# Performance work log

Measured on AMD Instinct MI355X. Metric: run time of the kernel, lower is better.

## Reference

```python
import jax, jax.numpy as jnp
import numpy as np

N = 20000      # nodes per batched graph
E = 320000     # directed edges per batched graph
F_IN = 128     # num_features
H = 256        # nhid == each gnn filter
G = 128        # number of graphs in batch


def setup_inputs() -> dict:
    key = jax.random.key(0)
    ks = jax.random.split(key, 24)

    def glorot(k, shape):
        fan_in, fan_out = shape[0], shape[1]
        limit = np.sqrt(6.0 / (fan_in + fan_out)).astype(np.float32)
        return jax.random.uniform(k, shape, jnp.float32, -limit, limit)

    inp = {
        'x1': jax.random.normal(ks[0], (N, F_IN), jnp.float32),
        'x2': jax.random.normal(ks[1], (N, F_IN), jnp.float32),
        'edge_index1': jax.random.randint(ks[2], (2, E), 0, N),
        'edge_index2': jax.random.randint(ks[3], (2, E), 0, N),
        'batch1': jnp.sort(jax.random.randint(ks[4], (N,), 0, G)),
        'batch2': jnp.sort(jax.random.randint(ks[5], (N,), 0, G)),
        # GCN layer weights (shared between the two graphs, as in the module)
        'W0': glorot(ks[6], (F_IN, H)), 'b0': jnp.zeros((H,), jnp.float32),
        'W1': glorot(ks[7], (H, H)),    'b1': jnp.zeros((H,), jnp.float32),
        'W2': glorot(ks[8], (H, H)),    'b2': jnp.zeros((H,), jnp.float32),
        # MLP head: nhid*2 -> nhid -> nhid//2 -> 1
        'lw0': glorot(ks[9], (2 * H, H)),      'lb0': jnp.zeros((H,), jnp.float32),
        'lw1': glorot(ks[10], (H, H // 2)),    'lb1': jnp.zeros((H // 2,), jnp.float32),
        'lw2': glorot(ks[11], (H // 2, 1)),    'lb2': jnp.zeros((1,), jnp.float32),
    }
    return inp


def _gcn_conv(x, src, dst, W, b, n):
    """PyG GCNConv: x' = D^-1/2 (A + I) D^-1/2 (x W) + b (self-loops added)."""
    x = x @ W                                      # [N, out]
    loop = jnp.arange(n)
    s = jnp.concatenate([src, loop])               # sources incl. self-loops
    d = jnp.concatenate([dst, loop])               # targets incl. self-loops
    deg = jax.ops.segment_sum(jnp.ones(s.shape, jnp.float32), d, num_segments=n)
    dinv = jnp.where(deg > 0, deg ** -0.5, 0.0)
    norm = dinv[s] * dinv[d]                       # [E+N]
    out = jax.ops.segment_sum(x[s] * norm[:, None], d, num_segments=n)
    return out + b


def _encode(x, edge_index, batch, params):
    src, dst = edge_index[0], edge_index[1]
    n = x.shape[0]
    for (W, b) in params:
        # conv -> relu -> dropout(eval: identity)
        x = jax.nn.relu(_gcn_conv(x, src, dst, W, b, n))
    # global_add_pool
    return jax.ops.segment_sum(x, batch, num_segments=G)   # [G, H]


def reference(x1, x2, W0, b0, W1, b1, W2, b2,
              lw0, lb0, lw1, lb1, lw2, lb2,
              edge_index1, edge_index2, batch1, batch2):
    params = ((W0, b0), (W1, b1), (W2, b2))
    g1 = _encode(x1, edge_index1, batch1, params)
    g2 = _encode(x2, edge_index2, batch2, params)
    scores = jnp.concatenate([g1, g2], axis=1)              # [G, 2H]
    h = jax.nn.relu(scores @ lw0 + lb0)
    h = jax.nn.relu(h @ lw1 + lb1)
    return jax.nn.sigmoid(h @ lw2 + lb2).reshape(-1)        # [G]
```

## Files before the change

### kernel.cpp

```cpp
#include <hip/hip_runtime.h>
#include <hip/hip_bf16.h>
#include <math.h>

#define HD 256
#define GB 128

typedef __attribute__((ext_vector_type(8))) short bf16x8;
typedef __attribute__((ext_vector_type(4))) float f32x4;

__device__ __forceinline__ float bf2f(unsigned short u) {
  return __uint_as_float(((unsigned int)u) << 16);
}
__device__ __forceinline__ unsigned short f2bf(float f) {
  unsigned int u = __float_as_uint(f);
  unsigned int r = u + 0x7FFFu + ((u >> 16) & 1u);
  return (unsigned short)(r >> 16);
}

__global__ void k_prep3(const float* __restrict__ W0, const float* __restrict__ W1,
                        const float* __restrict__ W2, unsigned short* __restrict__ Wt0,
                        unsigned short* __restrict__ Wt1, unsigned short* __restrict__ Wt2) {
  int i = blockIdx.x * blockDim.x + threadIdx.x;
  const float* W; unsigned short* Wt; int j;
  if (i < 32768)       { W = W0; Wt = Wt0; j = i; }
  else if (i < 98304)  { W = W1; Wt = Wt1; j = i - 32768; }
  else if (i < 163840) { W = W2; Wt = Wt2; j = i - 98304; }
  else return;
  int k = j >> 8, c = j & 255;
  Wt[(((size_t)(k >> 3) * HD) + c) * 8 + (k & 7)] = f2bf(W[(size_t)k * HD + c]);
}

__global__ void k_cvt2(const float4* __restrict__ in1, const float4* __restrict__ in2,
                       ushort4* __restrict__ out, int n4) {
  int i = blockIdx.x * blockDim.x + threadIdx.x;
  if (i >= 2 * n4) return;
  float4 v = (i < n4) ? in1[i] : in2[i - n4];
  ushort4 o;
  o.x = f2bf(v.x); o.y = f2bf(v.y); o.z = f2bf(v.z); o.w = f2bf(v.w);
  out[i] = o;
}

__global__ void k_zero(float* __restrict__ scores, int* __restrict__ deg, int ns, int nd) {
  int i = blockIdx.x * blockDim.x + threadIdx.x;
  if (i < ns) scores[i] = 0.f;
  else if (i < ns + nd) deg[i - ns] = 0;
}

__global__ void k_deg2(const int* __restrict__ dst1, const int* __restrict__ dst2,
                       int* __restrict__ deg, int e, int n0) {
  int i = blockIdx.x * blockDim.x + threadIdx.x;
  if (i >= 2 * e) return;
  int d = (i < e) ? dst1[i] : (dst2[i - e] + n0);
  atomicAdd(&deg[d], 1);
}

__global__ __launch_bounds__(256) void k_scan_a(const int* __restrict__ deg,
                                                int* __restrict__ partial, int n) {
  __shared__ int sh[256];
  int i = blockIdx.x * 256 + threadIdx.x;
  int v = (i < n) ? deg[i] : 0;
  sh[threadIdx.x] = v;
  __syncthreads();
#pragma unroll
  for (int off = 128; off; off >>= 1) {
    if (threadIdx.x < off) sh[threadIdx.x] += sh[threadIdx.x + off];
    __syncthreads();
  }
  if (threadIdx.x == 0) partial[blockIdx.x] = sh[0];
}

__global__ __launch_bounds__(256) void k_scan_b(int* __restrict__ partial, int nb,
                                                int* __restrict__ row_ptr, int n, int e_total) {
  __shared__ int sh[256];
  int t = threadIdx.x;
  int v = (t < nb) ? partial[t] : 0;
  sh[t] = v;
  __syncthreads();
#pragma unroll
  for (int off = 1; off < 256; off <<= 1) {
    int u = (t >= off) ? sh[t - off] : 0;
    __syncthreads();
    sh[t] += u;
    __syncthreads();
  }
  if (t < nb) partial[t] = sh[t] - v;
  if (t == 0) row_ptr[n] = e_total;
}

__global__ __launch_bounds__(256) void k_scan_c(const int* __restrict__ deg,
                                                const int* __restrict__ partial,
                                                int* __restrict__ row_ptr,
                                                float* __restrict__ dinv,
                                                int* __restrict__ cursor, int n) {
  __shared__ int sh[256];
  int i = blockIdx.x * 256 + threadIdx.x;
  int t = threadIdx.x;
  int v = (i < n) ? deg[i] : 0;
  sh[t] = v;
  __syncthreads();
#pragma unroll
  for (int off = 1; off < 256; off <<= 1) {
    int u = (t >= off) ? sh[t - off] : 0;
    __syncthreads();
    sh[t] += u;
    __syncthreads();
  }
  if (i < n) {
    row_ptr[i] = sh[t] - v + partial[blockIdx.x];
    dinv[i] = rsqrtf((float)(v + 1));
    cursor[i] = 0;
  }
}

__global__ void k_build2(const int* __restrict__ ei1, const int* __restrict__ ei2,
                         const float* __restrict__ dinv, const int* __restrict__ row_ptr,
                         int* __restrict__ cursor, int2* __restrict__ csr, int e, int n0) {
  int i = blockIdx.x * blockDim.x + threadIdx.x;
  if (i >= 2 * e) return;
  int s, d;
  if (i < e) { s = ei1[i];          d = ei1[i + e]; }
  else       { s = ei2[i - e] + n0; d = ei2[i] + n0; }
  int pos = atomicAdd(&cursor[d], 1);
  int idx = row_ptr[d] + pos;
  csr[idx] = make_int2(s, __float_as_int(dinv[s] * dinv[d]));
}

template<bool BR>
__global__ __launch_bounds__(256) void k_gemm_bf(const unsigned short* __restrict__ A,
                                                 const unsigned short* __restrict__ Wt,
                                                 const float* __restrict__ bias,
                                                 unsigned short* __restrict__ C,
                                                 int K) {
  const int w = threadIdx.x >> 6;
  const int lane = threadIdx.x & 63;
  const int bm = blockIdx.x * 64 + w * 16;
  const int bn = blockIdx.y * 128;
  const int row = bm + (lane & 15);
  const int kg0 = lane >> 4;
  f32x4 acc[8];
#pragma unroll
  for (int i = 0; i < 8; ++i) acc[i] = (f32x4){0.f, 0.f, 0.f, 0.f};

  const unsigned short* arow = A + (size_t)row * K + kg0 * 8;
  for (int k0 = 0; k0 < K; k0 += 32) {
    bf16x8 a = *(const bf16x8*)(arow + k0);
    const unsigned short* bbase =
        Wt + (((size_t)((k0 >> 3) + kg0) * HD) + bn + (lane & 15)) * 8;
#pragma unroll
    for (int nt = 0; nt < 8; ++nt) {
      bf16x8 b = *(const bf16x8*)(bbase + (size_t)nt * 16 * 8);
      acc[nt] = __builtin_amdgcn_mfma_f32_16x16x32_bf16(a, b, acc[nt], 0, 0, 0);
    }
  }
  const int crow = bm + (lane >> 4) * 4;
  const int ccol = bn + (lane & 15);
#pragma unroll
  for (int nt = 0; nt < 8; ++nt) {
    float bb = BR ? bias[ccol + nt * 16] : 0.f;
#pragma unroll
    for (int r = 0; r < 4; ++r) {
      float v = acc[nt][r];
      if (BR) v = fmaxf(v + bb, 0.f);
      C[(size_t)(crow + r) * HD + ccol + nt * 16] = f2bf(v);
    }
  }
}

template<int FB>
__device__ __forceinline__ void load_row(const unsigned short* p, float (&f)[FB]) {
  if constexpr (FB == 4) {
    ushort4 v = *(const ushort4*)p;
    f[0] = bf2f(v.x); f[1] = bf2f(v.y); f[2] = bf2f(v.z); f[3] = bf2f(v.w);
  } else {
    ushort2 v = *(const ushort2*)p;
    f[0] = bf2f(v.x); f[1] = bf2f(v.y);
  }
}

template<int FB, bool BR>
__global__ __launch_bounds__(256) void k_gath(const unsigned short* __restrict__ xw,
                                              const int* __restrict__ row_ptr,
                                              const int2* __restrict__ csr,
                                              const float* __restrict__ dinv,
                                              const float* __restrict__ bias,
                                              unsigned short* __restrict__ out, int n) {
  constexpr int F = FB * 64;
  int node = (blockIdx.x * blockDim.x + threadIdx.x) >> 6;
  int lane = threadIdx.x & 63;
  if (node >= n) return;
  float di = dinv[node];
  float c = di * di;
  float self[FB], acc0[FB], acc1[FB];
  load_row<FB>(xw + (size_t)node * F + lane * FB, self);
#pragma unroll
  for (int q = 0; q < FB; ++q) { acc0[q] = c * self[q]; acc1[q] = 0.f; }

  int e = row_ptr[node], end = row_ptr[node + 1];
  while (e < end) {
    int cnt = min(end - e, 64);
    int2 ew = make_int2(0, 0);
    if (lane < cnt) ew = csr[e + lane];
    int j = 0;
    for (; j + 4 <= cnt; j += 4) {
      int s0 = __shfl(ew.x, j + 0), s1 = __shfl(ew.x, j + 1);
      int s2 = __shfl(ew.x, j + 2), s3 = __shfl(ew.x, j + 3);
      float w0 = __int_as_float(__shfl(ew.y, j + 0));
      float w1 = __int_as_float(__shfl(ew.y, j + 1));
      float w2 = __int_as_float(__shfl(ew.y, j + 2));
      float w3 = __int_as_float(__shfl(ew.y, j + 3));
      float r0[FB], r1[FB], r2[FB], r3[FB];
      load_row<FB>(xw + (size_t)s0 * F + lane * FB, r0);
      load_row<FB>(xw + (size_t)s1 * F + lane * FB, r1);
      load_row<FB>(xw + (size_t)s2 * F + lane * FB, r2);
      load_row<FB>(xw + (size_t)s3 * F + lane * FB, r3);
#pragma unroll
      for (int q = 0; q < FB; ++q) {
        acc0[q] = fmaf(w0, r0[q], acc0[q]);
        acc1[q] = fmaf(w1, r1[q], acc1[q]);
        acc0[q] = fmaf(w2, r2[q], acc0[q]);
        acc1[q] = fmaf(w3, r3[q], acc1[q]);
      }
    }
    for (; j < cnt; ++j) {
      int s0 = __shfl(ew.x, j);
      float w0 = __int_as_float(__shfl(ew.y, j));
      float r0[FB];
      load_row<FB>(xw + (size_t)s0 * F + lane * FB, r0);
#pragma unroll
      for (int q = 0; q < FB; ++q) acc0[q] = fmaf(w0, r0[q], acc0[q]);
    }
    e += cnt;
  }
  unsigned short o[FB];
#pragma unroll
  for (int q = 0; q < FB; ++q) {
    float v = acc0[q] + acc1[q];
    if (BR) v = fmaxf(v + bias[lane * FB + q], 0.f);
    o[q] = f2bf(v);
  }
  if constexpr (FB == 4) {
    ushort4 ov; ov.x = o[0]; ov.y = o[1]; ov.z = o[2]; ov.w = o[3];
    *(ushort4*)(out + (size_t)node * F + lane * FB) = ov;
  } else {
    ushort2 ov; ov.x = o[0]; ov.y = o[1];
    *(ushort2*)(out + (size_t)node * F + lane * FB) = ov;
  }
}

__global__ __launch_bounds__(256) void k_pool4(const unsigned short* __restrict__ h,
                                               const int* __restrict__ batch1,
                                               const int* __restrict__ batch2,
                                               float* __restrict__ scores,
                                               int n, int n0) {
  int wave = (blockIdx.x * blockDim.x + threadIdx.x) >> 6;
  int lane = threadIdx.x & 63;
  int beg = wave * 32;
  if (beg >= n) return;
  int end = min(beg + 32, n);
  bool g1 = beg >= n0;
  const int* bat = g1 ? batch2 : batch1;
  int boff = g1 ? n0 : 0;
  int coff = g1 ? HD : 0;
  float ax = 0.f, ay = 0.f, az = 0.f, aw = 0.f;
  int cur = bat[beg - boff];
  for (int i = beg; i < end; ++i) {
    int b = bat[i - boff];
    if (b != cur) {
      float* srow = &scores[(size_t)cur * 512 + coff + lane * 4];
      atomicAdd(&srow[0], ax); atomicAdd(&srow[1], ay);
      atomicAdd(&srow[2], az); atomicAdd(&srow[3], aw);
      ax = ay = az = aw = 0.f;
      cur = b;
    }
    ushort4 v = reinterpret_cast<const ushort4*>(h + (size_t)i * HD)[lane];
    ax += bf2f(v.x); ay += bf2f(v.y); az += bf2f(v.z); aw += bf2f(v.w);
  }
  float* srow = &scores[(size_t)cur * 512 + coff + lane * 4];
  atomicAdd(&srow[0], ax); atomicAdd(&srow[1], ay);
  atomicAdd(&srow[2], az); atomicAdd(&srow[3], aw);
}

__global__ __launch_bounds__(256) void k_head_a(const float* __restrict__ scores,
                                                const float* __restrict__ lw0,
                                                const float* __restrict__ lb0,
                                                float* __restrict__ h1) {
  __shared__ float s_in[512];
  __shared__ float part[4][64];
  const int r = blockIdx.x, ct = blockIdx.y;
  const int t = threadIdx.x;
  s_in[t]       = scores[(size_t)r * 512 + t];
  s_in[t + 256] = scores[(size_t)r * 512 + t + 256];
  __syncthreads();
  const int l = t & 63, w = t >> 6;
  const int col = ct * 64 + l;
  float acc = 0.f;
  const float* wp = lw0 + (size_t)(w * 128) * 256 + col;
  const float* sp = s_in + w * 128;
#pragma unroll 8
  for (int k = 0; k < 128; ++k) acc = fmaf(sp[k], wp[(size_t)k * 256], acc);
  part[w][l] = acc;
  __syncthreads();
  if (t < 64) {
    float v = part[0][t] + part[1][t] + part[2][t] + part[3][t] + lb0[ct * 64 + t];
    h1[(size_t)r * 256 + ct * 64 + t] = fmaxf(v, 0.f);
  }
}

__global__ __launch_bounds__(256) void k_head_b(const float* __restrict__ h1,
                                                const float* __restrict__ lw1,
                                                const float* __restrict__ lb1,
                                                const float* __restrict__ lw2,
                                                const float* __restrict__ lb2,
                                                float* __restrict__ out) {
  __shared__ float s_in[256];
  __shared__ float part[2][128];
  __shared__ float s_h2[128];
  __shared__ float red[4];
  const int r = blockIdx.x;
  const int t = threadIdx.x;
  s_in[t] = h1[(size_t)r * 256 + t];
  __syncthreads();
  const int l = t & 127, w = t >> 7;
  float acc = 0.f;
  const float* wp = lw1 + (size_t)(w * 128) * 128 + l;
  const float* sp = s_in + w * 128;
#pragma unroll 8
  for (int k = 0; k < 128; ++k) acc = fmaf(sp[k], wp[(size_t)k * 128], acc);
  part[w][l] = acc;
  __syncthreads();
  if (t < 128) s_h2[t] = fmaxf(part[0][t] + part[1][t] + lb1[t], 0.f);
  __syncthreads();
  float p = (t < 128) ? s_h2[t] * lw2[t] : 0.f;
#pragma unroll
  for (int off = 32; off; off >>= 1) p += __shfl_down(p, off);
  if ((t & 63) == 0) red[t >> 6] = p;
  __syncthreads();
  if (t == 0) {
    float z = red[0] + red[1] + red[2] + red[3] + lb2[0];
    out[r] = 1.f / (1.f + expf(-z));
  }
}

extern "C" void kernel_launch(void* const* d_in, const int* in_sizes, int n_in,
                              void* d_out, int out_size, void* d_ws, size_t ws_size,
                              hipStream_t stream) {
  const float* x1 = (const float*)d_in[0];
  const float* x2 = (const float*)d_in[1];
  const int* ei1 = (const int*)d_in[2];
  const int* ei2 = (const int*)d_in[3];
  const int* batch1 = (const int*)d_in[4];
  const int* batch2 = (const int*)d_in[5];
  const float* W0 = (const float*)d_in[6];  const float* b0 = (const float*)d_in[7];
  const float* W1 = (const float*)d_in[8];  const float* b1 = (const float*)d_in[9];
  const float* W2 = (const float*)d_in[10]; const float* b2 = (const float*)d_in[11];
  const float* lw0 = (const float*)d_in[12]; const float* lb0 = (const float*)d_in[13];
  const float* lw1 = (const float*)d_in[14]; const float* lb1 = (const float*)d_in[15];
  const float* lw2 = (const float*)d_in[16]; const float* lb2 = (const float*)d_in[17];
  float* out = (float*)d_out;

  const int N = in_sizes[0] / 128;
  const int E = in_sizes[2] / 2;
  const int N2 = 2 * N, E2 = 2 * E;
  const int NB = (N2 + 255) / 256;

  char* p = (char*)d_ws;
  unsigned short* x_bf = (unsigned short*)p; p += (size_t)N2 * 128 * 2;
  unsigned short* aggx = (unsigned short*)p; p += (size_t)N2 * 128 * 2;
  unsigned short* buf0 = (unsigned short*)p; p += (size_t)N2 * HD * 2;
  unsigned short* buf1 = (unsigned short*)p; p += (size_t)N2 * HD * 2;
  unsigned short* Wt0  = (unsigned short*)p; p += (size_t)128 * HD * 2;
  unsigned short* Wt1  = (unsigned short*)p; p += (size_t)HD * HD * 2;
  unsigned short* Wt2  = (unsigned short*)p; p += (size_t)HD * HD * 2;
  float* dinv   = (float*)p; p += (size_t)N2 * 4;
  float* scores = (float*)p; p += (size_t)GB * 512 * 4;
  float* h1     = (float*)p; p += (size_t)GB * 256 * 4;
  int2* csr    = (int2*)p; p += (size_t)E2 * 8;
  int* deg     = (int*)p; p += (size_t)N2 * 4;
  int* row_ptr = (int*)p; p += (size_t)(N2 + 1) * 4;
  int* cursor  = (int*)p; p += (size_t)N2 * 4;
  int* partial = (int*)p; p += 256 * 4;

  k_prep3<<<(163840 + 255) / 256, 256, 0, stream>>>(W0, W1, W2, Wt0, Wt1, Wt2);
  int n4 = N * 128 / 4;
  k_cvt2<<<(2 * n4 + 255) / 256, 256, 0, stream>>>(
      (const float4*)x1, (const float4*)x2, (ushort4*)x_bf, n4);
  k_zero<<<(GB * 512 + N2 + 255) / 256, 256, 0, stream>>>(scores, deg, GB * 512, N2);

  k_deg2<<<(2 * E + 255) / 256, 256, 0, stream>>>(ei1 + E, ei2 + E, deg, E, N);
  k_scan_a<<<NB, 256, 0, stream>>>(deg, partial, N2);
  k_scan_b<<<1, 256, 0, stream>>>(partial, NB, row_ptr, N2, E2);
  k_scan_c<<<NB, 256, 0, stream>>>(deg, partial, row_ptr, dinv, cursor, N2);
  k_build2<<<(2 * E + 255) / 256, 256, 0, stream>>>(ei1, ei2, dinv, row_ptr,
                                                    cursor, csr, E, N);

  dim3 ggrid(N2 / 64, 2);
  k_gath<2, false><<<(N2 + 3) / 4, 256, 0, stream>>>(x_bf, row_ptr, csr, dinv,
                                                     nullptr, aggx, N2);
  k_gemm_bf<true><<<ggrid, 256, 0, stream>>>(aggx, Wt0, b0, buf0, 128);
  k_gemm_bf<false><<<ggrid, 256, 0, stream>>>(buf0, Wt1, nullptr, buf1, HD);
  k_gath<4, true><<<(N2 + 3) / 4, 256, 0, stream>>>(buf1, row_ptr, csr, dinv,
                                                    b1, buf0, N2);
  k_gemm_bf<false><<<ggrid, 256, 0, stream>>>(buf0, Wt2, nullptr, buf1, HD);
  k_gath<4, true><<<(N2 + 3) / 4, 256, 0, stream>>>(buf1, row_ptr, csr, dinv,
                                                    b2, buf0, N2);

  int waves = N2 / 32;
  k_pool4<<<(waves + 3) / 4, 256, 0, stream>>>(buf0, batch1, batch2, scores, N2, N);

  dim3 hgrid(GB, 4);
  k_head_a<<<hgrid, 256, 0, stream>>>(scores, lw0, lb0, h1);
  k_head_b<<<GB, 256, 0, stream>>>(h1, lw1, lb1, lw2, lb2, out);
}
```

Baseline: 273.3 us.

## Store gathered features in FP8 and fuse prep kernels into one launch

The inputs and the outputs of the per-layer GEMMs that feed the sparse gathers are now stored as FP8 (e4m3) instead of bf16. The gathers read them through packed fp8-to-f32 conversions, which halves the bytes moved in the bandwidth-bound neighbour aggregation. The weight transpose, input conversion and zero-init kernels are merged into one launch to cut launch overhead. The cost is much lower precision on activations (3 mantissa bits), which may push the output past the accuracy tolerance.

```diff
diff --git a/kernel.cpp b/kernel.cpp
--- a/kernel.cpp
+++ b/kernel.cpp
@@ -7,6 +7,7 @@
 
 typedef __attribute__((ext_vector_type(8))) short bf16x8;
 typedef __attribute__((ext_vector_type(4))) float f32x4;
+typedef __attribute__((ext_vector_type(2))) float f32x2;
 
 __device__ __forceinline__ float bf2f(unsigned short u) {
   return __uint_as_float(((unsigned int)u) << 16);
@@ -17,33 +18,81 @@
   return (unsigned short)(r >> 16);
 }
 
-__global__ void k_prep3(const float* __restrict__ W0, const float* __restrict__ W1,
-                        const float* __restrict__ W2, unsigned short* __restrict__ Wt0,
-                        unsigned short* __restrict__ Wt1, unsigned short* __restrict__ Wt2) {
+__device__ __forceinline__ float f8dec(unsigned u) {
+  unsigned s = (u >> 7) & 1u, e = (u >> 3) & 15u, m = u & 7u;
+  float mag = e ? __uint_as_float(((e + 120u) << 23) | (m << 20))
+                : (float)m * 0.001953125f;
+  return s ? -mag : mag;
+}
+__device__ __forceinline__ unsigned f8enc(float x) {
+#if __has_builtin(__builtin_amdgcn_cvt_pk_fp8_f32)
+  return (unsigned)__builtin_amdgcn_cvt_pk_fp8_f32(x, x, 0, false) & 0xFFu;
+#else
+  float a = fabsf(x);
+  unsigned s = x < 0.f ? 0x80u : 0u;
+  if (a >= 440.f) return s | 0x7Eu;
+  if (a < 0.015625f) {
+    int q = (int)rintf(a * 512.f);
+    return s | (unsigned)q;
+  }
+  unsigned u = __float_as_uint(a);
+  u += 0x7FFFFu + ((u >> 20) & 1u);
+  unsigned e = (u >> 23) - 120u;
+  if (e >= 16u) return s | 0x7Eu;
+  return s | (e << 3) | ((u >> 20) & 7u);
+#endif
+}
+
+template<int FB>
+__device__ __forceinline__ void load_row_f8(const unsigned char* p, float (&f)[FB]) {
+  if constexpr (FB == 4) {
+    unsigned u = *(const unsigned*)p;
+#if __has_builtin(__builtin_amdgcn_cvt_pk_f32_fp8)
+    f32x2 lo = __builtin_amdgcn_cvt_pk_f32_fp8((int)u, false);
+    f32x2 hi = __builtin_amdgcn_cvt_pk_f32_fp8((int)u, true);
+    f[0] = lo[0]; f[1] = lo[1]; f[2] = hi[0]; f[3] = hi[1];
+#else
+    f[0] = f8dec(u); f[1] = f8dec(u >> 8); f[2] = f8dec(u >> 16); f[3] = f8dec(u >> 24);
+#endif
+  } else {
+    unsigned u = *(const unsigned short*)p;
+#if __has_builtin(__builtin_amdgcn_cvt_pk_f32_fp8)
+    f32x2 lo = __builtin_amdgcn_cvt_pk_f32_fp8((int)u, false);
+    f[0] = lo[0]; f[1] = lo[1];
+#else
+    f[0] = f8dec(u); f[1] = f8dec(u >> 8);
+#endif
+  }
+}
+
+__global__ __launch_bounds__(256) void k_prep(const float* __restrict__ W0, const float* __restrict__ W1,
+                                              const float* __restrict__ W2,
+                                              unsigned short* __restrict__ Wt0,
+                                              unsigned short* __restrict__ Wt1,
+                                              unsigned short* __restrict__ Wt2,
+                                              const float4* __restrict__ x1, const float4* __restrict__ x2,
+                                              unsigned* __restrict__ x8, int n4,
+                                              float* __restrict__ scores, int* __restrict__ deg, int nd) {
   int i = blockIdx.x * blockDim.x + threadIdx.x;
-  const float* W; unsigned short* Wt; int j;
-  if (i < 32768)       { W = W0; Wt = Wt0; j = i; }
-  else if (i < 98304)  { W = W1; Wt = Wt1; j = i - 32768; }
-  else if (i < 163840) { W = W2; Wt = Wt2; j = i - 98304; }
-  else return;
-  int k = j >> 8, c = j & 255;
-  Wt[(((size_t)(k >> 3) * HD) + c) * 8 + (k & 7)] = f2bf(W[(size_t)k * HD + c]);
-}
-
-__global__ void k_cvt2(const float4* __restrict__ in1, const float4* __restrict__ in2,
-                       ushort4* __restrict__ out, int n4) {
-  int i = blockIdx.x * blockDim.x + threadIdx.x;
-  if (i >= 2 * n4) return;
-  float4 v = (i < n4) ? in1[i] : in2[i - n4];
-  ushort4 o;
-  o.x = f2bf(v.x); o.y = f2bf(v.y); o.z = f2bf(v.z); o.w = f2bf(v.w);
-  out[i] = o;
-}
-
-__global__ void k_zero(float* __restrict__ scores, int* __restrict__ deg, int ns, int nd) {
-  int i = blockIdx.x * blockDim.x + threadIdx.x;
-  if (i < ns) scores[i] = 0.f;
-  else if (i < ns + nd) deg[i - ns] = 0;
+  if (i < 163840) {
+    const float* W; unsigned short* Wt; int j;
+    if (i < 32768)      { W = W0; Wt = Wt0; j = i; }
+    else if (i < 98304) { W = W1; Wt = Wt1; j = i - 32768; }
+    else                { W = W2; Wt = Wt2; j = i - 98304; }
+    int k = j >> 8, c = j & 255;
+    Wt[(((size_t)(k >> 3) * HD) + c) * 8 + (k & 7)] = f2bf(W[(size_t)k * HD + c]);
+    return;
+  }
+  int j = i - 163840;
+  if (j < 2 * n4) {
+    float4 v = (j < n4) ? x1[j] : x2[j - n4];
+    x8[j] = f8enc(v.x) | (f8enc(v.y) << 8) | (f8enc(v.z) << 16) | (f8enc(v.w) << 24);
+    return;
+  }
+  j -= 2 * n4;
+  if (j < GB * 512) { scores[j] = 0.f; return; }
+  j -= GB * 512;
+  if (j < nd) deg[j] = 0;
 }
 
 __global__ void k_deg2(const int* __restrict__ dst1, const int* __restrict__ dst2,
@@ -125,11 +174,11 @@
   csr[idx] = make_int2(s, __float_as_int(dinv[s] * dinv[d]));
 }
 
-template<bool BR>
+template<bool BR, bool F8OUT>
 __global__ __launch_bounds__(256) void k_gemm_bf(const unsigned short* __restrict__ A,
                                                  const unsigned short* __restrict__ Wt,
                                                  const float* __restrict__ bias,
-                                                 unsigned short* __restrict__ C,
+                                                 void* __restrict__ Cv,
                                                  int K) {
   const int w = threadIdx.x >> 6;
   const int lane = threadIdx.x & 63;
@@ -161,29 +210,20 @@
     for (int r = 0; r < 4; ++r) {
       float v = acc[nt][r];
       if (BR) v = fmaxf(v + bb, 0.f);
-      C[(size_t)(crow + r) * HD + ccol + nt * 16] = f2bf(v);
+      size_t idx = (size_t)(crow + r) * HD + ccol + nt * 16;
+      if constexpr (F8OUT) ((unsigned char*)Cv)[idx] = (unsigned char)f8enc(v);
+      else                 ((unsigned short*)Cv)[idx] = f2bf(v);
     }
   }
 }
 
-template<int FB>
-__device__ __forceinline__ void load_row(const unsigned short* p, float (&f)[FB]) {
-  if constexpr (FB == 4) {
-    ushort4 v = *(const ushort4*)p;
-    f[0] = bf2f(v.x); f[1] = bf2f(v.y); f[2] = bf2f(v.z); f[3] = bf2f(v.w);
-  } else {
-    ushort2 v = *(const ushort2*)p;
-    f[0] = bf2f(v.x); f[1] = bf2f(v.y);
-  }
-}
-
 template<int FB, bool BR>
-__global__ __launch_bounds__(256) void k_gath(const unsigned short* __restrict__ xw,
-                                              const int* __restrict__ row_ptr,
-                                              const int2* __restrict__ csr,
-                                              const float* __restrict__ dinv,
-                                              const float* __restrict__ bias,
-                                              unsigned short* __restrict__ out, int n) {
+__global__ __launch_bounds__(256) void k_gathf8(const unsigned char* __restrict__ y,
+                                                const int* __restrict__ row_ptr,
+                                                const int2* __restrict__ csr,
+                                                const float* __restrict__ dinv,
+                                                const float* __restrict__ bias,
+                                                unsigned short* __restrict__ out, int n) {
   constexpr int F = FB * 64;
   int node = (blockIdx.x * blockDim.x + threadIdx.x) >> 6;
   int lane = threadIdx.x & 63;
@@ -191,7 +231,7 @@
   float di = dinv[node];
   float c = di * di;
   float self[FB], acc0[FB], acc1[FB];
-  load_row<FB>(xw + (size_t)node * F + lane * FB, self);
+  load_row_f8<FB>(y + (size_t)node * F + lane * FB, self);
 #pragma unroll
   for (int q = 0; q < FB; ++q) { acc0[q] = c * self[q]; acc1[q] = 0.f; }
 
@@ -209,10 +249,10 @@
       float w2 = __int_as_float(__shfl(ew.y, j + 2));
       float w3 = __int_as_float(__shfl(ew.y, j + 3));
       float r0[FB], r1[FB], r2[FB], r3[FB];
-      load_row<FB>(xw + (size_t)s0 * F + lane * FB, r0);
-      load_row<FB>(xw + (size_t)s1 * F + lane * FB, r1);
-      load_row<FB>(xw + (size_t)s2 * F + lane * FB, r2);
-      load_row<FB>(xw + (size_t)s3 * F + lane * FB, r3);
+      load_row_f8<FB>(y + (size_t)s0 * F + lane * FB, r0);
+      load_row_f8<FB>(y + (size_t)s1 * F + lane * FB, r1);
+      load_row_f8<FB>(y + (size_t)s2 * F + lane * FB, r2);
+      load_row_f8<FB>(y + (size_t)s3 * F + lane * FB, r3);
 #pragma unroll
       for (int q = 0; q < FB; ++q) {
         acc0[q] = fmaf(w0, r0[q], acc0[q]);
@@ -225,7 +265,7 @@
       int s0 = __shfl(ew.x, j);
       float w0 = __int_as_float(__shfl(ew.y, j));
       float r0[FB];
-      load_row<FB>(xw + (size_t)s0 * F + lane * FB, r0);
+      load_row_f8<FB>(y + (size_t)s0 * F + lane * FB, r0);
 #pragma unroll
       for (int q = 0; q < FB; ++q) acc0[q] = fmaf(w0, r0[q], acc0[q]);
     }
@@ -364,10 +404,10 @@
   const int NB = (N2 + 255) / 256;
 
   char* p = (char*)d_ws;
-  unsigned short* x_bf = (unsigned short*)p; p += (size_t)N2 * 128 * 2;
+  unsigned char*  x8   = (unsigned char*)p;  p += (size_t)N2 * 128;
   unsigned short* aggx = (unsigned short*)p; p += (size_t)N2 * 128 * 2;
-  unsigned short* buf0 = (unsigned short*)p; p += (size_t)N2 * HD * 2;
-  unsigned short* buf1 = (unsigned short*)p; p += (size_t)N2 * HD * 2;
+  unsigned short* h    = (unsigned short*)p; p += (size_t)N2 * HD * 2;
+  unsigned char*  y    = (unsigned char*)p;  p += (size_t)N2 * HD;
   unsigned short* Wt0  = (unsigned short*)p; p += (size_t)128 * HD * 2;
   unsigned short* Wt1  = (unsigned short*)p; p += (size_t)HD * HD * 2;
   unsigned short* Wt2  = (unsigned short*)p; p += (size_t)HD * HD * 2;
@@ -380,11 +420,11 @@
   int* cursor  = (int*)p; p += (size_t)N2 * 4;
   int* partial = (int*)p; p += 256 * 4;
 
-  k_prep3<<<(163840 + 255) / 256, 256, 0, stream>>>(W0, W1, W2, Wt0, Wt1, Wt2);
   int n4 = N * 128 / 4;
-  k_cvt2<<<(2 * n4 + 255) / 256, 256, 0, stream>>>(
-      (const float4*)x1, (const float4*)x2, (ushort4*)x_bf, n4);
-  k_zero<<<(GB * 512 + N2 + 255) / 256, 256, 0, stream>>>(scores, deg, GB * 512, N2);
+  int prep_total = 163840 + 2 * n4 + GB * 512 + N2;
+  k_prep<<<(prep_total + 255) / 256, 256, 0, stream>>>(
+      W0, W1, W2, Wt0, Wt1, Wt2,
+      (const float4*)x1, (const float4*)x2, (unsigned*)x8, n4, scores, deg, N2);
 
   k_deg2<<<(2 * E + 255) / 256, 256, 0, stream>>>(ei1 + E, ei2 + E, deg, E, N);
   k_scan_a<<<NB, 256, 0, stream>>>(deg, partial, N2);
@@ -394,18 +434,18 @@
                                                     cursor, csr, E, N);
 
   dim3 ggrid(N2 / 64, 2);
-  k_gath<2, false><<<(N2 + 3) / 4, 256, 0, stream>>>(x_bf, row_ptr, csr, dinv,
-                                                     nullptr, aggx, N2);
-  k_gemm_bf<true><<<ggrid, 256, 0, stream>>>(aggx, Wt0, b0, buf0, 128);
-  k_gemm_bf<false><<<ggrid, 256, 0, stream>>>(buf0, Wt1, nullptr, buf1, HD);
-  k_gath<4, true><<<(N2 + 3) / 4, 256, 0, stream>>>(buf1, row_ptr, csr, dinv,
-                                                    b1, buf0, N2);
-  k_gemm_bf<false><<<ggrid, 256, 0, stream>>>(buf0, Wt2, nullptr, buf1, HD);
-  k_gath<4, true><<<(N2 + 3) / 4, 256, 0, stream>>>(buf1, row_ptr, csr, dinv,
-                                                    b2, buf0, N2);
+  k_gathf8<2, false><<<(N2 + 3) / 4, 256, 0, stream>>>(x8, row_ptr, csr, dinv,
+                                                       nullptr, aggx, N2);
+  k_gemm_bf<true, false><<<ggrid, 256, 0, stream>>>(aggx, Wt0, b0, h, 128);
+  k_gemm_bf<false, true><<<ggrid, 256, 0, stream>>>(h, Wt1, nullptr, y, HD);
+  k_gathf8<4, true><<<(N2 + 3) / 4, 256, 0, stream>>>(y, row_ptr, csr, dinv,
+                                                      b1, h, N2);
+  k_gemm_bf<false, true><<<ggrid, 256, 0, stream>>>(h, Wt2, nullptr, y, HD);
+  k_gathf8<4, true><<<(N2 + 3) / 4, 256, 0, stream>>>(y, row_ptr, csr, dinv,
+                                                      b2, h, N2);
 
   int waves = N2 / 32;
-  k_pool4<<<(waves + 3) / 4, 256, 0, stream>>>(buf0, batch1, batch2, scores, N2, N);
+  k_pool4<<<(waves + 3) / 4, 256, 0, stream>>>(h, batch1, batch2, scores, N2, N);
 
   dim3 hgrid(GB, 4);
   k_head_a<<<hgrid, 256, 0, stream>>>(scores, lw0, lb0, h1);
```

Result: faster. 239.3 us (median of 2 runs) (-12.5%).
